# Kernel optimization log

Measured on AMD Instinct MI355X. Metric: run time of the kernel, lower is better.

The kernel has to match this reference:

```python
import jax, jax.numpy as jnp
import numpy as np

B, IN_C, IN_L, T = 8, 64, 64, 256
OUT_C, OUT_L = 64, 64
KH, KW = 3, 3
K = IN_C * KH * KW  # 576
EPS = 1e-5


def setup_inputs() -> dict:
    key = jax.random.key(0)
    k1, k2 = jax.random.split(key, 2)
    x = jax.random.normal(k1, (B, IN_C, IN_L, T), dtype=jnp.float32)
    # xavier-normal-ish scale for fan_in = K
    weight = jax.random.normal(k2, (K, OUT_C, OUT_L), dtype=jnp.float32) * (1.0 / np.sqrt(K))
    bias = jnp.zeros((OUT_C, OUT_L), dtype=jnp.float32)
    gamma = jnp.ones((OUT_C,), dtype=jnp.float32)
    beta = jnp.zeros((OUT_C,), dtype=jnp.float32)
    alpha = jnp.full((1,), 0.25, dtype=jnp.float32)  # PReLU single-parameter init
    return {"x": x, "weight": weight, "bias": bias, "gamma": gamma, "beta": beta, "alpha": alpha}


def _unfold3x3(x):
    # torch nn.Unfold(kernel=(3,3), stride=1, padding=1): output channel index = c*9 + i*3 + j
    xp = jnp.pad(x, ((0, 0), (0, 0), (1, 1), (1, 1)))
    pats = jnp.stack([xp[:, :, i:i + IN_L, j:j + T] for i in range(KH) for j in range(KW)], axis=2)  # (B, C, 9, L, T)
    return pats.reshape(x.shape[0], K, IN_L, T)


def reference(x, weight, bias, gamma, beta, alpha):
    patches = _unfold3x3(x)  # (B, K, L, T); out_l_unfold == in_l, out_t == t, so slicing is a no-op
    # locally-connected conv: per out_l position weight, shared over time
    out = jnp.einsum('bklt,kcl->bclt', patches, weight)  # (B, out_c, out_l, T)
    out = out + bias[None, :, :, None]
    # BatchNorm2d (training mode: batch statistics, biased variance)
    mean = out.mean(axis=(0, 2, 3), keepdims=True)
    var = out.var(axis=(0, 2, 3), keepdims=True)
    out = (out - mean) * jax.lax.rsqrt(var + EPS) * gamma[None, :, None, None] + beta[None, :, None, None]
    # PReLU with single shared parameter
    return jnp.where(out >= 0, out, alpha[0] * out)
```

## Files before the change

### kernel.cpp

```cpp
#include <hip/hip_runtime.h>

typedef __attribute__((ext_vector_type(8))) short short8;
typedef __attribute__((ext_vector_type(8))) unsigned short ushort8;
typedef __attribute__((ext_vector_type(4))) float f32x4;

constexpr int B_ = 8, IN_C_ = 64, IN_L_ = 64, T_ = 256, OUT_C_ = 64, OUT_L_ = 64;
constexpr float EPS_ = 1e-5f;

constexpr int XT_LP = 66, XT_TP = 258, XT_IC = 64;
constexpr int XT_LSTRIDE = XT_TP * XT_IC;
constexpr int XT_BSTRIDE = XT_LP * XT_LSTRIDE;
constexpr size_t XT_ELEMS = (size_t)B_ * XT_BSTRIDE;
constexpr size_t XT_BYTES = XT_ELEMS * 2;
constexpr size_t WT2_ELEMS = 64ull * 9 * 64 * 64;
constexpr size_t WT2_OFF_B = XT_BYTES;
constexpr size_t PART_OFF_B = WT2_OFF_B + WT2_ELEMS * 2;
constexpr size_t PART_BYTES = 1024ull * 128 * 4;
constexpr size_t TMP_OFF_B = PART_OFF_B + PART_BYTES;
constexpr size_t TMP_BYTES = (size_t)B_ * OUT_C_ * OUT_L_ * T_ * 2;
constexpr size_t WS_NEED = TMP_OFF_B;
constexpr size_t WS_NEED2 = TMP_OFF_B + TMP_BYTES;

__device__ __forceinline__ unsigned short f2bf(float f) {
  unsigned u = __float_as_uint(f);
  return (unsigned short)((u + 0x7fffu + ((u >> 16) & 1u)) >> 16);
}

__device__ __forceinline__ void gload_lds16(const void* g, void* l) {
  __builtin_amdgcn_global_load_lds(
      (const __attribute__((address_space(1))) unsigned int*)g,
      (__attribute__((address_space(3))) unsigned int*)l, 16, 0, 0);
}

__global__ __launch_bounds__(256) void prep_kernel(const float* __restrict__ x,
                                                   const float* __restrict__ w,
                                                   unsigned short* __restrict__ xT,
                                                   unsigned short* __restrict__ wT2) {
  const int bid = blockIdx.x;
  const int tid = threadIdx.x;
  __shared__ unsigned char shmem[34816];
  if (bid < 144) {
    const int tap = bid >> 4;
    const int c0 = (bid & 15) * 4;
    auto wls = (unsigned short(*)[4][68])shmem;
    {
      const int ic = tid >> 2, cl = tid & 3;
      const float* src = w + (((size_t)(ic * 9 + tap) * 64) + (c0 + cl)) * 64;
#pragma unroll
      for (int e = 0; e < 16; ++e) {
        float4 v = ((const float4*)src)[e];
        const int l = e * 4;
        wls[l + 0][cl][ic] = f2bf(v.x);
        wls[l + 1][cl][ic] = f2bf(v.y);
        wls[l + 2][cl][ic] = f2bf(v.z);
        wls[l + 3][cl][ic] = f2bf(v.w);
      }
    }
    __syncthreads();
    {
      const int l = tid >> 2, cl = tid & 3;
      const unsigned short* row = &wls[l][cl][0];
      uint4* dst = (uint4*)(wT2 + ((size_t)(l * 9 + tap)) * 4096 + (c0 + cl) * 64);
#pragma unroll
      for (int q = 0; q < 8; ++q) dst[q] = ((const uint4*)row)[q];
    }
  } else if (bid < 1168) {
    const int u = bid - 144;
    const int th = u & 1, l = (u >> 1) & 63, b = u >> 7;
    const int t0 = th * 128;
    auto ls = (unsigned short(*)[132])shmem;
    {
      const int ic = tid >> 2, q = tid & 3;
      const float4* src = (const float4*)(x + (((size_t)(b * 64 + ic) * 64 + l) * 256 + t0));
#pragma unroll
      for (int e = 0; e < 8; ++e) {
        float4 v = src[q * 8 + e];
        const int toff = (q * 8 + e) * 4;
        unsigned d0 = f2bf(v.x) | ((unsigned)f2bf(v.y) << 16);
        unsigned d1 = f2bf(v.z) | ((unsigned)f2bf(v.w) << 16);
        *(uint2*)&ls[ic][toff] = make_uint2(d0, d1);
      }
    }
    __syncthreads();
    {
      const int tl = tid >> 1, h = tid & 1;
      unsigned d[16];
#pragma unroll
      for (int k = 0; k < 16; ++k) {
        unsigned short a = ls[h * 32 + 2 * k][tl];
        unsigned short c = ls[h * 32 + 2 * k + 1][tl];
        d[k] = a | ((unsigned)c << 16);
      }
      unsigned short* dst =
          xT + ((size_t)(b * XT_LP + l + 1) * XT_TP + (t0 + tl + 1)) * XT_IC + h * 32;
      uint4* dv = (uint4*)dst;
      dv[0] = make_uint4(d[0], d[1], d[2], d[3]);
      dv[1] = make_uint4(d[4], d[5], d[6], d[7]);
      dv[2] = make_uint4(d[8], d[9], d[10], d[11]);
      dv[3] = make_uint4(d[12], d[13], d[14], d[15]);
    }
  } else {
    const int b = bid - 1168;
    unsigned short* base = xT + (size_t)b * XT_BSTRIDE;
    const short8 z = {};
    for (int ci = tid; ci < 5184; ci += 256) {
      size_t off;
      if (ci < 4128) {
        const int plane = ci / 2064, k = ci % 2064;
        off = (size_t)(plane ? 65 : 0) * XT_LSTRIDE + (size_t)k * 8;
      } else {
        const int k = ci - 4128;
        const int lp = k >> 4, rem = k & 15;
        const int tp = (rem < 8) ? 0 : 257;
        off = ((size_t)lp * XT_TP + tp) * 64 + (size_t)(rem & 7) * 8;
      }
      *(short8*)(base + off) = z;
    }
  }
}

__global__ __launch_bounds__(256, 2) void conv_mfma(
    const unsigned short* __restrict__ xT, const unsigned short* __restrict__ wT2,
    const float* __restrict__ bias, float* __restrict__ outf,
    unsigned short* __restrict__ tmpb, float* __restrict__ part) {
  const int orig = blockIdx.x;
  const int xcd = orig & 7;
  const int idx = orig >> 3;
  const int b = idx >> 4;
  const int th = (idx >> 3) & 1;
  const int l = xcd * 8 + (idx & 7);
  const int wg = ((b << 6) + l) * 2 + th;
  const int tid = threadIdx.x;
  const int wid = tid >> 6, ln = tid & 63;
  const int lc = ln & 15, lg = ln >> 4;
  const int m0 = wid * 32;
  const int tp0 = th * 128;

  __shared__ unsigned short Al[26624];
  __shared__ unsigned short Bl[2][4096];

  {
    const unsigned short* rbase = xT + ((size_t)(b * XT_LP + l) * XT_TP + tp0) * 64;
#pragma unroll
    for (int k = 0; k < 13; ++k) {
      const int cbase = k * 256 + wid * 64;
      const int ci = cbase + ln;
      const int i = ci / 1040;
      const int r = ci - i * 1040;
      const int d = r >> 3, s = r & 7;
      gload_lds16(rbase + (size_t)i * XT_LSTRIDE + d * 64 + ((s ^ (d & 7)) << 3),
                  Al + (size_t)cbase * 8);
    }
  }
  const unsigned short* wBase = wT2 + (size_t)l * 9 * 4096;
  auto BSTAGE = [&](int buf, int tap) {
#pragma unroll
    for (int q = 0; q < 2; ++q) {
      const int cbase = q * 256 + wid * 64;
      const int ci = cbase + ln;
      const int crow = ci >> 3, s = ci & 7;
      gload_lds16(wBase + (size_t)tap * 4096 + crow * 64 + ((s ^ (crow & 7)) << 3),
                  &Bl[buf][0] + (size_t)cbase * 8);
    }
  };

  f32x4 acc[2][4] = {};

  BSTAGE(0, 0);
  __syncthreads();

#pragma unroll
  for (int tap = 0; tap < 9; ++tap) {
    __builtin_amdgcn_s_barrier();
    if (tap + 1 < 9) {
      BSTAGE((tap + 1) & 1, tap + 1);
      asm volatile("s_waitcnt vmcnt(2)" ::: "memory");
    } else {
      asm volatile("s_waitcnt vmcnt(0)" ::: "memory");
    }
    __builtin_amdgcn_sched_barrier(0);
    __builtin_amdgcn_s_barrier();
    __builtin_amdgcn_sched_barrier(0);

    const int i = tap / 3, j = tap - (tap / 3) * 3;
    const unsigned short* Lb = &Bl[tap & 1][0];
#pragma unroll
    for (int kb = 0; kb < 2; ++kb) {
      short8 af[2], bf[4];
#pragma unroll
      for (int mi = 0; mi < 2; ++mi) {
        const int d = m0 + mi * 16 + lc + j;
        af[mi] = *(const short8*)(Al + (i * 130 + d) * 64 +
                                  (((kb * 4 + lg) ^ (d & 7)) << 3));
      }
#pragma unroll
      for (int ni = 0; ni < 4; ++ni)
        bf[ni] = *(const short8*)(Lb + (ni * 16 + lc) * 64 +
                                  (((kb * 4 + lg) ^ (lc & 7)) << 3));
#pragma unroll
      for (int mi = 0; mi < 2; ++mi)
#pragma unroll
        for (int ni = 0; ni < 4; ++ni)
          acc[mi][ni] =
              __builtin_amdgcn_mfma_f32_16x16x32_bf16(af[mi], bf[ni], acc[mi][ni], 0, 0, 0);
    }
  }

  __syncthreads();
  float* sm = (float*)&Al[0];
#pragma unroll
  for (int ni = 0; ni < 4; ++ni) {
    const int c = ni * 16 + lc;
    const float bv = bias[c * 64 + l];
    float s = 0.f, s2 = 0.f;
    const size_t obase = ((size_t)(b * 64 + c) * 64 + l) * 256 + tp0 + m0;
#pragma unroll
    for (int mi = 0; mi < 2; ++mi) {
      float vv[4];
#pragma unroll
      for (int r = 0; r < 4; ++r) {
        float v = acc[mi][ni][r] + bv;
        vv[r] = v;
        s += v;
        s2 += v * v;
      }
      if (tmpb) {
        unsigned d0 = f2bf(vv[0]) | ((unsigned)f2bf(vv[1]) << 16);
        unsigned d1 = f2bf(vv[2]) | ((unsigned)f2bf(vv[3]) << 16);
        *(uint2*)(tmpb + obase + mi * 16 + lg * 4) = make_uint2(d0, d1);
      } else {
        *(float4*)(outf + obase + mi * 16 + lg * 4) =
            make_float4(vv[0], vv[1], vv[2], vv[3]);
      }
    }
    s += __shfl_xor(s, 16);  s += __shfl_xor(s, 32);
    s2 += __shfl_xor(s2, 16); s2 += __shfl_xor(s2, 32);
    if (lg == 0) {
      sm[(wid * 4 + ni) * 32 + lc * 2] = s;
      sm[(wid * 4 + ni) * 32 + lc * 2 + 1] = s2;
    }
  }
  __syncthreads();
  if (tid < 128) {
    const int sel = tid >> 6, cc = tid & 63;
    const int ni = cc >> 4, lc2 = cc & 15;
    float r = 0.f;
#pragma unroll
    for (int w2 = 0; w2 < 4; ++w2) r += sm[(w2 * 4 + ni) * 32 + lc2 * 2 + sel];
    part[(size_t)wg * 128 + sel * 64 + cc] = r;
  }
}

__global__ __launch_bounds__(256) void bn_stats_prelu_b(
    const float* __restrict__ part, const float* __restrict__ gamma,
    const float* __restrict__ beta, const float* __restrict__ alpha,
    const unsigned short* __restrict__ tmp, float* __restrict__ out) {
  const int c = blockIdx.x >> 5;
  const int seg = blockIdx.x & 31;
  const int tid = threadIdx.x;
  float s = 0.f, s2 = 0.f;
  for (int i = tid; i < 1024; i += 256) {
    s += part[(size_t)i * 128 + c];
    s2 += part[(size_t)i * 128 + 64 + c];
  }
#pragma unroll
  for (int off = 32; off; off >>= 1) {
    s += __shfl_down(s, off);
    s2 += __shfl_down(s2, off);
  }
  __shared__ float r0[4], r1[4];
  const int wid = tid >> 6, lane = tid & 63;
  if (lane == 0) { r0[wid] = s; r1[wid] = s2; }
  __syncthreads();
  const float S = r0[0] + r0[1] + r0[2] + r0[3];
  const float S2 = r1[0] + r1[1] + r1[2] + r1[3];
  const float inv_n = 1.0f / 131072.f;
  const float mean = S * inv_n;
  const float var = S2 * inv_n - mean * mean;
  const float sc = gamma[c] * rsqrtf(var + EPS_);
  const float sh = beta[c] - mean * sc;
  const float a = alpha[0];
  const size_t base8 = ((size_t)((seg >> 2) * 64 + c)) * 2048 + (size_t)(seg & 3) * 512;
#pragma unroll 2
  for (int k = tid; k < 512; k += 256) {
    const size_t i = base8 + k;
    ushort8 v = *(const ushort8*)(tmp + i * 8);
    float o[8];
#pragma unroll
    for (int r = 0; r < 8; ++r) {
      float f = __uint_as_float(((unsigned)v[r]) << 16) * sc + sh;
      o[r] = (f >= 0.f) ? f : a * f;
    }
    float4* op = (float4*)(out + i * 8);
    op[0] = make_float4(o[0], o[1], o[2], o[3]);
    op[1] = make_float4(o[4], o[5], o[6], o[7]);
  }
}

__global__ __launch_bounds__(256) void bn_stats_prelu_f(
    const float* __restrict__ part, const float* __restrict__ gamma,
    const float* __restrict__ beta, const float* __restrict__ alpha,
    float* __restrict__ out) {
  const int c = blockIdx.x >> 5;
  const int seg = blockIdx.x & 31;
  const int tid = threadIdx.x;
  float s = 0.f, s2 = 0.f;
  for (int i = tid; i < 1024; i += 256) {
    s += part[(size_t)i * 128 + c];
    s2 += part[(size_t)i * 128 + 64 + c];
  }
#pragma unroll
  for (int off = 32; off; off >>= 1) {
    s += __shfl_down(s, off);
    s2 += __shfl_down(s2, off);
  }
  __shared__ float r0[4], r1[4];
  const int wid = tid >> 6, lane = tid & 63;
  if (lane == 0) { r0[wid] = s; r1[wid] = s2; }
  __syncthreads();
  const float S = r0[0] + r0[1] + r0[2] + r0[3];
  const float S2 = r1[0] + r1[1] + r1[2] + r1[3];
  const float inv_n = 1.0f / 131072.f;
  const float mean = S * inv_n;
  const float var = S2 * inv_n - mean * mean;
  const float sc = gamma[c] * rsqrtf(var + EPS_);
  const float sh = beta[c] - mean * sc;
  const float a = alpha[0];
  const size_t base4 = ((size_t)((seg >> 2) * 64 + c)) * 4096 + (size_t)(seg & 3) * 1024;
  for (int k = tid; k < 1024; k += 256) {
    float4 v = ((float4*)out)[base4 + k];
    v.x = v.x * sc + sh; v.x = (v.x >= 0.f) ? v.x : a * v.x;
    v.y = v.y * sc + sh; v.y = (v.y >= 0.f) ? v.y : a * v.y;
    v.z = v.z * sc + sh; v.z = (v.z >= 0.f) ? v.z : a * v.z;
    v.w = v.w * sc + sh; v.w = (v.w >= 0.f) ? v.w : a * v.w;
    ((float4*)out)[base4 + k] = v;
  }
}

extern "C" void kernel_launch(void* const* d_in, const int* in_sizes, int n_in,
                              void* d_out, int out_size, void* d_ws, size_t ws_size,
                              hipStream_t stream) {
  const float* x = (const float*)d_in[0];
  const float* w = (const float*)d_in[1];
  const float* bias = (const float*)d_in[2];
  const float* gamma = (const float*)d_in[3];
  const float* beta = (const float*)d_in[4];
  const float* alpha = (const float*)d_in[5];
  float* out = (float*)d_out;

  unsigned short* xT = (unsigned short*)d_ws;
  unsigned short* wT2 = (unsigned short*)((char*)d_ws + WT2_OFF_B);
  float* part = (float*)((char*)d_ws + PART_OFF_B);

  if (ws_size >= WS_NEED2) {
    unsigned short* tmpb = (unsigned short*)((char*)d_ws + TMP_OFF_B);
    prep_kernel<<<dim3(1176), dim3(256), 0, stream>>>(x, w, xT, wT2);
    conv_mfma<<<dim3(1024), dim3(256), 0, stream>>>(xT, wT2, bias, out, tmpb, part);
    bn_stats_prelu_b<<<dim3(2048), dim3(256), 0, stream>>>(part, gamma, beta, alpha, tmpb, out);
  } else if (ws_size >= WS_NEED) {
    prep_kernel<<<dim3(1176), dim3(256), 0, stream>>>(x, w, xT, wT2);
    conv_mfma<<<dim3(1024), dim3(256), 0, stream>>>(xT, wT2, bias, out, nullptr, part);
    bn_stats_prelu_f<<<dim3(2048), dim3(256), 0, stream>>>(part, gamma, beta, alpha, out);
  }
}
```

Measured before the change: 61.30 us.

## Double each conv workgroup's tile to full time axis and stream A per tap

Each conv workgroup now covers the full 256-step time range for one (batch, l) pair instead of half of it, so the grid drops from 1024 to 512 blocks and each wave computes a 64x64 tile with a 4x4 accumulator array. The whole padded input slab is no longer preloaded into LDS. For each tap, the shifted 256x64 A slice and the 64x64 weight slice are streamed into double-buffered LDS, reusing one XOR swizzle for both. This raises MFMA work per LDS read of B and halves the partial-statistics buffer. In exchange it uses more registers and re-fetches overlapping input rows for every tap, and with only 512 blocks there may not be enough to fill the GPU.

```diff
diff --git a/kernel.cpp b/kernel.cpp
--- a/kernel.cpp
+++ b/kernel.cpp
@@ -15,7 +15,7 @@
 constexpr size_t WT2_ELEMS = 64ull * 9 * 64 * 64;
 constexpr size_t WT2_OFF_B = XT_BYTES;
 constexpr size_t PART_OFF_B = WT2_OFF_B + WT2_ELEMS * 2;
-constexpr size_t PART_BYTES = 1024ull * 128 * 4;
+constexpr size_t PART_BYTES = 512ull * 128 * 4;
 constexpr size_t TMP_OFF_B = PART_OFF_B + PART_BYTES;
 constexpr size_t TMP_BYTES = (size_t)B_ * OUT_C_ * OUT_L_ * T_ * 2;
 constexpr size_t WS_NEED = TMP_OFF_B;
@@ -124,57 +124,46 @@
     const float* __restrict__ bias, float* __restrict__ outf,
     unsigned short* __restrict__ tmpb, float* __restrict__ part) {
   const int orig = blockIdx.x;
-  const int xcd = orig & 7;
-  const int idx = orig >> 3;
-  const int b = idx >> 4;
-  const int th = (idx >> 3) & 1;
-  const int l = xcd * 8 + (idx & 7);
-  const int wg = ((b << 6) + l) * 2 + th;
+  const int wg = (orig >> 6) * 64 + (orig & 7) * 8 + ((orig >> 3) & 7);
+  const int b = wg >> 6, l = wg & 63;
   const int tid = threadIdx.x;
   const int wid = tid >> 6, ln = tid & 63;
   const int lc = ln & 15, lg = ln >> 4;
-  const int m0 = wid * 32;
-  const int tp0 = th * 128;
-
-  __shared__ unsigned short Al[26624];
-  __shared__ unsigned short Bl[2][4096];
-
-  {
-    const unsigned short* rbase = xT + ((size_t)(b * XT_LP + l) * XT_TP + tp0) * 64;
-#pragma unroll
-    for (int k = 0; k < 13; ++k) {
-      const int cbase = k * 256 + wid * 64;
-      const int ci = cbase + ln;
-      const int i = ci / 1040;
-      const int r = ci - i * 1040;
-      const int d = r >> 3, s = r & 7;
-      gload_lds16(rbase + (size_t)i * XT_LSTRIDE + d * 64 + ((s ^ (d & 7)) << 3),
-                  Al + (size_t)cbase * 8);
-    }
-  }
-  const unsigned short* wBase = wT2 + (size_t)l * 9 * 4096;
-  auto BSTAGE = [&](int buf, int tap) {
+  const int m0 = wid * 64;
+
+  __shared__ unsigned short lds[2][20480];
+
+  const int src_lane_off = ((ln >> 3) << 6) + ((((ln & 7) ^ (ln >> 3))) << 3);
+  const unsigned short* xBase = xT + (size_t)(b * XT_LP + l) * XT_LSTRIDE + src_lane_off;
+  const unsigned short* wBase = wT2 + (size_t)l * 9 * 4096 + src_lane_off;
+
+  auto STAGE = [&](int buf, int tap) {
+    const int i = tap / 3, j = tap - i * 3;
+    const unsigned short* Ab = xBase + (size_t)i * XT_LSTRIDE + j * 64;
+    unsigned short* La = &lds[buf][0];
+#pragma unroll
+    for (int q = 0; q < 8; ++q) {
+      const int ch = wid * 8 + q;
+      gload_lds16(Ab + ch * 512, La + ch * 512);
+    }
+    const unsigned short* Bb = wBase + (size_t)tap * 4096;
+    unsigned short* Lb = &lds[buf][16384];
 #pragma unroll
     for (int q = 0; q < 2; ++q) {
-      const int cbase = q * 256 + wid * 64;
-      const int ci = cbase + ln;
-      const int crow = ci >> 3, s = ci & 7;
-      gload_lds16(wBase + (size_t)tap * 4096 + crow * 64 + ((s ^ (crow & 7)) << 3),
-                  &Bl[buf][0] + (size_t)cbase * 8);
+      const int ch = wid * 2 + q;
+      gload_lds16(Bb + ch * 512, Lb + ch * 512);
     }
   };
 
-  f32x4 acc[2][4] = {};
-
-  BSTAGE(0, 0);
-  __syncthreads();
-
+  f32x4 acc[4][4] = {};
+
+  STAGE(0, 0);
 #pragma unroll
   for (int tap = 0; tap < 9; ++tap) {
     __builtin_amdgcn_s_barrier();
     if (tap + 1 < 9) {
-      BSTAGE((tap + 1) & 1, tap + 1);
-      asm volatile("s_waitcnt vmcnt(2)" ::: "memory");
+      STAGE((tap + 1) & 1, tap + 1);
+      asm volatile("s_waitcnt vmcnt(10)" ::: "memory");
     } else {
       asm volatile("s_waitcnt vmcnt(0)" ::: "memory");
     }
@@ -182,23 +171,20 @@
     __builtin_amdgcn_s_barrier();
     __builtin_amdgcn_sched_barrier(0);
 
-    const int i = tap / 3, j = tap - (tap / 3) * 3;
-    const unsigned short* Lb = &Bl[tap & 1][0];
+    const unsigned short* La = &lds[tap & 1][0];
+    const unsigned short* Lb = &lds[tap & 1][16384];
 #pragma unroll
     for (int kb = 0; kb < 2; ++kb) {
-      short8 af[2], bf[4];
-#pragma unroll
-      for (int mi = 0; mi < 2; ++mi) {
-        const int d = m0 + mi * 16 + lc + j;
-        af[mi] = *(const short8*)(Al + (i * 130 + d) * 64 +
-                                  (((kb * 4 + lg) ^ (d & 7)) << 3));
-      }
+      const int slot = (((kb * 4 + lg) ^ (lc & 7)) << 3);
+      short8 af[4], bf[4];
+#pragma unroll
+      for (int mi = 0; mi < 4; ++mi)
+        af[mi] = *(const short8*)(La + (m0 + mi * 16 + lc) * 64 + slot);
 #pragma unroll
       for (int ni = 0; ni < 4; ++ni)
-        bf[ni] = *(const short8*)(Lb + (ni * 16 + lc) * 64 +
-                                  (((kb * 4 + lg) ^ (lc & 7)) << 3));
-#pragma unroll
-      for (int mi = 0; mi < 2; ++mi)
+        bf[ni] = *(const short8*)(Lb + (ni * 16 + lc) * 64 + slot);
+#pragma unroll
+      for (int mi = 0; mi < 4; ++mi)
 #pragma unroll
         for (int ni = 0; ni < 4; ++ni)
           acc[mi][ni] =
@@ -207,15 +193,15 @@
   }
 
   __syncthreads();
-  float* sm = (float*)&Al[0];
+  float* sm = (float*)&lds[0][0];
 #pragma unroll
   for (int ni = 0; ni < 4; ++ni) {
     const int c = ni * 16 + lc;
     const float bv = bias[c * 64 + l];
     float s = 0.f, s2 = 0.f;
-    const size_t obase = ((size_t)(b * 64 + c) * 64 + l) * 256 + tp0 + m0;
-#pragma unroll
-    for (int mi = 0; mi < 2; ++mi) {
+    const size_t obase = ((size_t)(b * 64 + c) * 64 + l) * 256 + m0;
+#pragma unroll
+    for (int mi = 0; mi < 4; ++mi) {
       float vv[4];
 #pragma unroll
       for (int r = 0; r < 4; ++r) {
@@ -259,7 +245,7 @@
   const int seg = blockIdx.x & 31;
   const int tid = threadIdx.x;
   float s = 0.f, s2 = 0.f;
-  for (int i = tid; i < 1024; i += 256) {
+  for (int i = tid; i < 512; i += 256) {
     s += part[(size_t)i * 128 + c];
     s2 += part[(size_t)i * 128 + 64 + c];
   }
@@ -305,7 +291,7 @@
   const int seg = blockIdx.x & 31;
   const int tid = threadIdx.x;
   float s = 0.f, s2 = 0.f;
-  for (int i = tid; i < 1024; i += 256) {
+  for (int i = tid; i < 512; i += 256) {
     s += part[(size_t)i * 128 + c];
     s2 += part[(size_t)i * 128 + 64 + c];
   }
@@ -355,11 +341,11 @@
   if (ws_size >= WS_NEED2) {
     unsigned short* tmpb = (unsigned short*)((char*)d_ws + TMP_OFF_B);
     prep_kernel<<<dim3(1176), dim3(256), 0, stream>>>(x, w, xT, wT2);
-    conv_mfma<<<dim3(1024), dim3(256), 0, stream>>>(xT, wT2, bias, out, tmpb, part);
+    conv_mfma<<<dim3(512), dim3(256), 0, stream>>>(xT, wT2, bias, out, tmpb, part);
     bn_stats_prelu_b<<<dim3(2048), dim3(256), 0, stream>>>(part, gamma, beta, alpha, tmpb, out);
   } else if (ws_size >= WS_NEED) {
     prep_kernel<<<dim3(1176), dim3(256), 0, stream>>>(x, w, xT, wT2);
-    conv_mfma<<<dim3(1024), dim3(256), 0, stream>>>(xT, wT2, bias, out, nullptr, part);
+    conv_mfma<<<dim3(512), dim3(256), 0, stream>>>(xT, wT2, bias, out, nullptr, part);
     bn_stats_prelu_f<<<dim3(2048), dim3(256), 0, stream>>>(part, gamma, beta, alpha, out);
   }
 }
```

Result: faster. 53.42 us (-12.9%).
